# Performance work log

Hardware: AMD Instinct MI355X
Metric: run time of the kernel (lower is better)

The kernel has to match this reference:

```python
import jax, jax.numpy as jnp
import numpy as np

N, E, F_IN, H, C = 50000, 800000, 128, 64, 10

def setup_inputs() -> dict:
    key = jax.random.key(0)
    ks = jax.random.split(key, 8)
    x = jax.random.normal(ks[0], (N, F_IN), dtype=jnp.float32)
    edge_index = jax.random.randint(ks[1], (2, E), 0, N, dtype=jnp.int32)
    edge_weight = jax.random.uniform(ks[2], (E,), dtype=jnp.float32)
    W1 = jax.random.normal(ks[3], (H, F_IN), dtype=jnp.float32) * 0.05
    W2 = jax.random.normal(ks[4], (H, H), dtype=jnp.float32) * 0.05
    W3 = jax.random.normal(ks[5], (C, H), dtype=jnp.float32) * 0.05
    b1 = jnp.zeros((H,), jnp.float32)
    b2 = jnp.zeros((H,), jnp.float32)
    b3 = jnp.zeros((C,), jnp.float32)
    return {"x": x, "edge_index": edge_index, "edge_weight": edge_weight,
            "W1": W1, "b1": b1, "W2": W2, "b2": b2, "W3": W3, "b3": b3}

def reference(x, edge_index, edge_weight, W1, b1, W2, b2, W3, b3):
    n = x.shape[0]
    row, col = edge_index[0], edge_index[1]
    # GCN symmetric normalization (add_self_loops=False): deg from edge weights on col
    deg = jax.ops.segment_sum(edge_weight, col, num_segments=n)  # [N]
    dinv = jnp.where(deg > 0, jax.lax.rsqrt(deg), 0.0)
    norm = dinv[row] * edge_weight * dinv[col]  # [E]

    def gcn_layer(h, W, b):
        h = h @ W.T                               # linear transform [N, out]
        msg = h[row] * norm[:, None]              # gather + scale   [E, out]
        agg = jax.ops.segment_sum(msg, col, num_segments=n)  # scatter-add [N, out]
        return agg + b

    h = gcn_layer(x, W1, b1)
    h = gcn_layer(h, W2, b2)
    logits = gcn_layer(h, W3, b3)
    soft = jax.nn.softmax(logits, axis=1)
    return logits, soft
```

## Files before the change

kernel.cpp:

```cpp
#include <hip/hip_runtime.h>
#include <hip/hip_fp16.h>

#define N_NODES 50000
#define N_EDGES 800000
#define F_IN    128
#define H_DIM   64
#define C_DIM   10
#define CPAD    16
#define CAP     48
#define BLOCK   256
#define BIN_NODES 256
#define NBINS   196
#define QN      64
#define STRIDE  4480
#define E_BLK   2048
#define ABLOCKS ((N_EDGES + E_BLK - 1) / E_BLK)
#define DGB     (N_NODES / 16)
#define WB      ((N_NODES * 64) / 256)
#define POISON  ((int)0xAAAAAAAA)

__device__ __forceinline__ int unbase(int v) {
    return ((unsigned)v < 65536u) ? v : v - POISON;
}

__device__ __forceinline__ int   prow(unsigned v) { return (int)(v >> 16); }
__device__ __forceinline__ float pw(unsigned v)   {
    return __half2float(__ushort_as_half((unsigned short)(v & 0xFFFFu)));
}

__global__ __launch_bounds__(256) void k_binA(const int* __restrict__ rows,
                                              const int* __restrict__ cols,
                                              const float* __restrict__ ew,
                                              const float* __restrict__ W1,
                                              const float* __restrict__ b1,
                                              const float* __restrict__ W2,
                                              const float* __restrict__ b2,
                                              const float* __restrict__ W3,
                                              int* __restrict__ bucketCnt,
                                              unsigned* __restrict__ regionA,
                                              unsigned short* __restrict__ regionC,
                                              float* __restrict__ T2g,
                                              float* __restrict__ v1g,
                                              float* __restrict__ v2g) {
    const int tid = threadIdx.x;
    if (blockIdx.x < ABLOCKS) {
        __shared__ unsigned       sA[E_BLK];
        __shared__ unsigned short sC[E_BLK];
        __shared__ int hcnt[NBINS];
        __shared__ int lbase[NBINS];
        __shared__ int gb[NBINS];
        for (int i = tid; i < NBINS; i += BLOCK) hcnt[i] = 0;
        __syncthreads();

        const int e0 = blockIdx.x * E_BLK;
        unsigned rw[8];
        unsigned cl[8];
#pragma unroll
        for (int j = 0; j < 8; ++j) {
            int e = e0 + j * BLOCK + tid;
            if (e < N_EDGES) {
                int   c = cols[e];
                int   r = rows[e];
                float w = ew[e];
                rw[j] = ((unsigned)r << 16) | (unsigned)__half_as_ushort(__float2half(w));
                int lr = atomicAdd(&hcnt[c >> 8], 1);
                cl[j] = (unsigned)c | ((unsigned)lr << 16);
            } else {
                cl[j] = 0xFFFFFFFFu;
            }
        }
        __syncthreads();

        if (tid < 64) {
            int run = 0;
            for (int base = 0; base < NBINS; base += 64) {
                int i = base + tid;
                int v = (i < NBINS) ? hcnt[i] : 0;
                int s = v;
#pragma unroll
                for (int off = 1; off < 64; off <<= 1) {
                    int t = __shfl_up(s, off);
                    if (tid >= off) s += t;
                }
                if (i < NBINS) lbase[i] = run + s - v;
                run += __shfl(s, 63);
            }
        }
        __syncthreads();

#pragma unroll
        for (int j = 0; j < 8; ++j) {
            if (cl[j] != 0xFFFFFFFFu) {
                int c  = (int)(cl[j] & 0xFFFFu);
                int lr = (int)(cl[j] >> 16);
                int pos = lbase[c >> 8] + lr;
                sA[pos] = rw[j];
                sC[pos] = (unsigned short)c;
            }
        }
        if (tid < NBINS && hcnt[tid] > 0)
            gb[tid] = unbase(atomicAdd(&bucketCnt[tid], hcnt[tid]));
        __syncthreads();

        const int total = lbase[NBINS - 1] + hcnt[NBINS - 1];
        for (int i = tid; i < total; i += BLOCK) {
            int c = sC[i];
            int b = c >> 8;
            int gpos = gb[b] + (i - lbase[b]);
            if (gpos < STRIDE) {
                size_t p = (size_t)b * STRIDE + gpos;
                regionA[p] = sA[i];
                regionC[p] = (unsigned short)c;
            }
        }
        return;
    }

    __shared__ float u[C_DIM * H_DIM];
    for (int idx = tid; idx < C_DIM * H_DIM; idx += BLOCK) {
        int c = idx >> 6, j = idx & 63;
        float a = 0.f;
#pragma unroll
        for (int k = 0; k < H_DIM; ++k) a += W3[c * H_DIM + k] * W2[k * H_DIM + j];
        u[idx] = a;
    }
    __syncthreads();
    for (int idx = tid; idx < C_DIM * F_IN; idx += BLOCK) {
        int c = idx >> 7, f = idx & 127;
        float a = 0.f;
#pragma unroll
        for (int k = 0; k < H_DIM; ++k) a += u[c * H_DIM + k] * W1[k * F_IN + f];
        T2g[idx] = a;
    }
    if (tid < C_DIM) {
        float a = 0.f, b = 0.f;
#pragma unroll
        for (int k = 0; k < H_DIM; ++k) {
            a += u[tid * H_DIM + k] * b1[k];
            b += W3[tid * H_DIM + k] * b2[k];
        }
        v1g[tid] = a;
        v2g[tid] = b;
    }
}

__global__ __launch_bounds__(256) void k_binB(const int* __restrict__ bucketCnt,
                                              const unsigned* __restrict__ regionA,
                                              const unsigned short* __restrict__ regionC,
                                              float2* __restrict__ meta,
                                              unsigned* __restrict__ edata) {
    __shared__ unsigned sdata[QN * CAP];
    __shared__ int   lcnt[QN];
    __shared__ float wsum[QN];
    const int tid = threadIdx.x;
    const int b   = blockIdx.x >> 2;
    const int q   = blockIdx.x & 3;
    const int n0  = b * BIN_NODES + q * QN;
    if (n0 >= N_NODES) return;
    if (tid < QN) { lcnt[tid] = 0; wsum[tid] = 0.f; }
    __syncthreads();

    int tot = unbase(bucketCnt[b]);
    if (tot > STRIDE) tot = STRIDE;
    const size_t segBase = (size_t)b * STRIDE;
    const int lo = q * QN, hi = lo + QN;
    for (int i = tid; i < tot; i += BLOCK) {
        int cl = (int)regionC[segBase + i] - b * BIN_NODES;
        unsigned e = regionA[segBase + i];
        if (cl >= lo && cl < hi) {
            int nl = cl - lo;
            int r = atomicAdd(&lcnt[nl], 1);
            if (r < CAP) sdata[nl * CAP + r] = e;
            atomicAdd(&wsum[nl], pw(e));
        }
    }
    __syncthreads();

    const int nvalid = min(N_NODES - n0, QN);
    if (tid < nvalid) {
        int c0 = min(lcnt[tid], CAP);
        int cp = (c0 + 15) & ~15;
        if (cp > CAP) cp = CAP;
        for (int r = c0; r < cp; ++r) sdata[tid * CAP + r] = 0u;
        float d = wsum[tid];
        meta[n0 + tid] = make_float2(d > 0.f ? rsqrtf(d) : 0.f, (float)cp);
    }
    __syncthreads();

    int4* dst = reinterpret_cast<int4*>(edata + (size_t)n0 * CAP);
    const int4* src = reinterpret_cast<const int4*>(sdata);
    const int nvec = nvalid * (CAP / 4);
    for (int i = tid; i < nvec; i += BLOCK) dst[i] = src[i];
}

__global__ __launch_bounds__(256) void k_dg(const float* __restrict__ x,
                                            const float* __restrict__ T2g,
                                            const float2* __restrict__ meta,
                                            __half* __restrict__ bufA) {
    __shared__ float ts[16 * 132];
    __shared__ float xs[16][132];
    const int tid = threadIdx.x;
    const int n0 = blockIdx.x * 16;

    for (int i = tid; i < 16 * F_IN; i += BLOCK) {
        int c = i >> 7;
        ts[c * 132 + (i & 127)] = (c < C_DIM) ? T2g[i] : 0.f;
    }
    for (int i = tid; i < 16 * 32; i += BLOCK) {
        int ln = i >> 5, f4 = i & 31;
        float4 v = reinterpret_cast<const float4*>(x)[(n0 + ln) * 32 + f4];
        *reinterpret_cast<float4*>(&xs[ln][f4 * 4]) = v;
    }
    __syncthreads();

    const int g = tid >> 4;
    const int c = tid & 15;
    const int n = n0 + g;
    const float di = meta[n].x;

    const float4* tsv = reinterpret_cast<const float4*>(&ts[c * 132]);
    const float4* xv  = reinterpret_cast<const float4*>(&xs[g][0]);
    float a = 0.f;
#pragma unroll 8
    for (int f4 = 0; f4 < 32; ++f4) {
        float4 xx = xv[f4], tt = tsv[f4];
        a += xx.x * tt.x + xx.y * tt.y + xx.z * tt.z + xx.w * tt.w;
    }
    float outv = (c < C_DIM) ? a * di : (c == 10 ? di : 0.f);
    bufA[n * CPAD + c] = __float2half(outv);
}

__global__ __launch_bounds__(256) void k_gather(const float2* __restrict__ meta,
                                                const unsigned* __restrict__ edata,
                                                const __half* __restrict__ zin,
                                                __half* __restrict__ zout) {
    int n = (blockIdx.x * 256 + threadIdx.x) >> 6;
    if (n >= N_NODES) return;
    const int lane = threadIdx.x & 63;
    const int sub = lane >> 3;
    const int c2  = lane & 7;
    float2 m = meta[n];
    const float di = m.x;
    const int iters = ((int)m.y) >> 4;
    const uint2* bp = reinterpret_cast<const uint2*>(edata + n * CAP) + sub;
    float ax = 0.f, ay = 0.f;
#pragma unroll
    for (int i = 0; i < 3; ++i) {
        if (i < iters) {
            uint2 e = bp[i * 8];
            {
                float2 z = __half22float2(
                    reinterpret_cast<const __half2*>(zin + prow(e.x) * CPAD)[c2]);
                float w = pw(e.x);
                ax += w * z.x; ay += w * z.y;
            }
            {
                float2 z = __half22float2(
                    reinterpret_cast<const __half2*>(zin + prow(e.y) * CPAD)[c2]);
                float w = pw(e.y);
                ax += w * z.x; ay += w * z.y;
            }
        }
    }
    ax += __shfl_xor(ax, 8);  ay += __shfl_xor(ay, 8);
    ax += __shfl_xor(ax, 16); ay += __shfl_xor(ay, 16);
    ax += __shfl_xor(ax, 32); ay += __shfl_xor(ay, 32);
    if (lane < 8) {
        float s = di * di;
        reinterpret_cast<__half2*>(zout + n * CPAD)[lane] =
            __floats2half2_rn(ax * s, ay * s);
    }
}

__global__ __launch_bounds__(256) void k_final(const float2* __restrict__ meta,
                                               const unsigned* __restrict__ edata,
                                               const __half* __restrict__ zin,
                                               const __half* __restrict__ s1buf,
                                               const float* __restrict__ v1,
                                               const float* __restrict__ v2,
                                               const float* __restrict__ b3,
                                               float* __restrict__ logits,
                                               float* __restrict__ soft) {
    int n = (blockIdx.x * 256 + threadIdx.x) >> 6;
    if (n >= N_NODES) return;
    const int lane = threadIdx.x & 63;
    const int sub = lane >> 3;
    const int c2  = lane & 7;
    float2 m = meta[n];
    const float di = m.x;
    const int iters = ((int)m.y) >> 4;
    const uint2* bp = reinterpret_cast<const uint2*>(edata + n * CAP) + sub;
    float ax = 0.f, ay = 0.f;
#pragma unroll
    for (int i = 0; i < 3; ++i) {
        if (i < iters) {
            uint2 e = bp[i * 8];
            {
                float2 z = __half22float2(
                    reinterpret_cast<const __half2*>(zin + prow(e.x) * CPAD)[c2]);
                float w = pw(e.x);
                ax += w * z.x; ay += w * z.y;
            }
            {
                float2 z = __half22float2(
                    reinterpret_cast<const __half2*>(zin + prow(e.y) * CPAD)[c2]);
                float w = pw(e.y);
                ax += w * z.x; ay += w * z.y;
            }
        }
    }
    ax += __shfl_xor(ax, 8);  ay += __shfl_xor(ay, 8);
    ax += __shfl_xor(ax, 16); ay += __shfl_xor(ay, 16);
    ax += __shfl_xor(ax, 32); ay += __shfl_xor(ay, 32);

    const float r  = di > 0.f ? 1.0f / di : 0.f;
    const float a1 = __half2float(s1buf[n * CPAD + 10]) * r;
    const float a2 = __half2float(zin[n * CPAD + 10]) * r;
    float l0 = -1e30f, l1 = -1e30f;
    if (c2 < 5) {
        float2 w1 = reinterpret_cast<const float2*>(v1)[c2];
        float2 w2 = reinterpret_cast<const float2*>(v2)[c2];
        float2 bb = reinterpret_cast<const float2*>(b3)[c2];
        l0 = di * ax + a2 * w1.x + a1 * w2.x + bb.x;
        l1 = di * ay + a2 * w1.y + a1 * w2.y + bb.y;
    }
    float mx = fmaxf(l0, l1);
    mx = fmaxf(mx, __shfl_xor(mx, 1));
    mx = fmaxf(mx, __shfl_xor(mx, 2));
    mx = fmaxf(mx, __shfl_xor(mx, 4));
    float e0 = (c2 < 5) ? __expf(l0 - mx) : 0.f;
    float e1 = (c2 < 5) ? __expf(l1 - mx) : 0.f;
    float s = e0 + e1;
    s += __shfl_xor(s, 1);
    s += __shfl_xor(s, 2);
    s += __shfl_xor(s, 4);
    if (lane < 5) {
        float inv = 1.0f / s;
        reinterpret_cast<float2*>(logits + (size_t)n * C_DIM)[lane] = make_float2(l0, l1);
        reinterpret_cast<float2*>(soft   + (size_t)n * C_DIM)[lane] = make_float2(e0 * inv, e1 * inv);
    }
}

extern "C" void kernel_launch(void* const* d_in, const int* in_sizes, int n_in,
                              void* d_out, int out_size, void* d_ws, size_t ws_size,
                              hipStream_t stream) {
    const float* x  = (const float*)d_in[0];
    const int*   ei = (const int*)d_in[1];
    const float* ew = (const float*)d_in[2];
    const float* W1 = (const float*)d_in[3];
    const float* b1 = (const float*)d_in[4];
    const float* W2 = (const float*)d_in[5];
    const float* b2 = (const float*)d_in[6];
    const float* W3 = (const float*)d_in[7];
    const float* b3 = (const float*)d_in[8];
    const int* rows = ei;
    const int* cols = ei + N_EDGES;

    char* ws = (char*)d_ws;
    size_t off = 0;
    auto alloc = [&](size_t bytes) { void* q = ws + off; off += (bytes + 15) & ~size_t(15); return q; };

    float2*         meta      = (float2*)         alloc((size_t)N_NODES * 8);
    __half*         bufA      = (__half*)         alloc((size_t)N_NODES * CPAD * 2);
    __half*         bufB      = (__half*)         alloc((size_t)N_NODES * CPAD * 2);
    float*          T2g       = (float*)          alloc(C_DIM * F_IN * 4);
    float*          v1        = (float*)          alloc(64);
    float*          v2        = (float*)          alloc(64);
    int*            bucketCnt = (int*)            alloc(NBINS * 4);
    unsigned*       regionA   = (unsigned*)       alloc((size_t)NBINS * STRIDE * 4);
    unsigned short* regionC   = (unsigned short*) alloc((size_t)NBINS * STRIDE * 2);
    unsigned*       edata     = (unsigned*)       alloc((size_t)N_NODES * CAP * 4);

    float* logits = (float*)d_out;
    float* soft   = logits + N_NODES * C_DIM;

    k_binA<<<ABLOCKS + 1, BLOCK, 0, stream>>>(rows, cols, ew, W1, b1, W2, b2, W3,
                                              bucketCnt, regionA, regionC, T2g, v1, v2);
    k_binB<<<NBINS * 4, BLOCK, 0, stream>>>(bucketCnt, regionA, regionC, meta, edata);
    k_dg<<<DGB, BLOCK, 0, stream>>>(x, T2g, meta, bufA);
    k_gather<<<WB, BLOCK, 0, stream>>>(meta, edata, bufA, bufB);
    k_gather<<<WB, BLOCK, 0, stream>>>(meta, edata, bufB, bufA);
    k_final<<<WB, BLOCK, 0, stream>>>(meta, edata, bufA, bufB, v1, v2, b3,
                                      logits, soft);
}
```

Baseline: 167.9 us.

## Fuse feature projection into binning kernel and grid-stride gather kernels

Moves the x·T2 projection (former k_dg) into k_binB, so each bin block computes the projected features for its 64 nodes using the dinv it just computed in shared memory. This removes one kernel launch and the meta re-read. Separately, the gather and final kernels switch from one wave per node to a fixed 2048-block grid-stride loop, which cuts block scheduling overhead. The cost is extra shared memory and serial work per binB block, which may reduce occupancy in that kernel.

```diff
diff --git a/kernel.cpp b/kernel.cpp
--- a/kernel.cpp
+++ b/kernel.cpp
@@ -15,8 +15,8 @@
 #define STRIDE  4480
 #define E_BLK   2048
 #define ABLOCKS ((N_EDGES + E_BLK - 1) / E_BLK)
-#define DGB     (N_NODES / 16)
-#define WB      ((N_NODES * 64) / 256)
+#define GBLK    2048
+#define NWAVES  (GBLK * 4)
 #define POISON  ((int)0xAAAAAAAA)
 
 __device__ __forceinline__ int unbase(int v) {
@@ -147,17 +147,27 @@
 __global__ __launch_bounds__(256) void k_binB(const int* __restrict__ bucketCnt,
                                               const unsigned* __restrict__ regionA,
                                               const unsigned short* __restrict__ regionC,
+                                              const float* __restrict__ x,
+                                              const float* __restrict__ T2g,
                                               float2* __restrict__ meta,
-                                              unsigned* __restrict__ edata) {
+                                              unsigned* __restrict__ edata,
+                                              __half* __restrict__ bufA) {
     __shared__ unsigned sdata[QN * CAP];
     __shared__ int   lcnt[QN];
     __shared__ float wsum[QN];
+    __shared__ float dinvs[QN];
+    __shared__ float ts[16 * 132];
+    __shared__ float xs[16][132];
     const int tid = threadIdx.x;
     const int b   = blockIdx.x >> 2;
     const int q   = blockIdx.x & 3;
     const int n0  = b * BIN_NODES + q * QN;
     if (n0 >= N_NODES) return;
     if (tid < QN) { lcnt[tid] = 0; wsum[tid] = 0.f; }
+    for (int i = tid; i < 16 * F_IN; i += BLOCK) {
+        int c = i >> 7;
+        ts[c * 132 + (i & 127)] = (c < C_DIM) ? T2g[i] : 0.f;
+    }
     __syncthreads();
 
     int tot = unbase(bucketCnt[b]);
@@ -183,92 +193,88 @@
         if (cp > CAP) cp = CAP;
         for (int r = c0; r < cp; ++r) sdata[tid * CAP + r] = 0u;
         float d = wsum[tid];
-        meta[n0 + tid] = make_float2(d > 0.f ? rsqrtf(d) : 0.f, (float)cp);
+        float di = d > 0.f ? rsqrtf(d) : 0.f;
+        dinvs[tid] = di;
+        meta[n0 + tid] = make_float2(di, (float)cp);
     }
     __syncthreads();
 
-    int4* dst = reinterpret_cast<int4*>(edata + (size_t)n0 * CAP);
-    const int4* src = reinterpret_cast<const int4*>(sdata);
-    const int nvec = nvalid * (CAP / 4);
-    for (int i = tid; i < nvec; i += BLOCK) dst[i] = src[i];
-}
-
-__global__ __launch_bounds__(256) void k_dg(const float* __restrict__ x,
-                                            const float* __restrict__ T2g,
-                                            const float2* __restrict__ meta,
-                                            __half* __restrict__ bufA) {
-    __shared__ float ts[16 * 132];
-    __shared__ float xs[16][132];
-    const int tid = threadIdx.x;
-    const int n0 = blockIdx.x * 16;
-
-    for (int i = tid; i < 16 * F_IN; i += BLOCK) {
-        int c = i >> 7;
-        ts[c * 132 + (i & 127)] = (c < C_DIM) ? T2g[i] : 0.f;
-    }
-    for (int i = tid; i < 16 * 32; i += BLOCK) {
-        int ln = i >> 5, f4 = i & 31;
-        float4 v = reinterpret_cast<const float4*>(x)[(n0 + ln) * 32 + f4];
-        *reinterpret_cast<float4*>(&xs[ln][f4 * 4]) = v;
-    }
-    __syncthreads();
-
-    const int g = tid >> 4;
-    const int c = tid & 15;
-    const int n = n0 + g;
-    const float di = meta[n].x;
-
-    const float4* tsv = reinterpret_cast<const float4*>(&ts[c * 132]);
-    const float4* xv  = reinterpret_cast<const float4*>(&xs[g][0]);
-    float a = 0.f;
+    {
+        int4* dst = reinterpret_cast<int4*>(edata + (size_t)n0 * CAP);
+        const int4* src = reinterpret_cast<const int4*>(sdata);
+        const int nvec = nvalid * (CAP / 4);
+        for (int i = tid; i < nvec; i += BLOCK) dst[i] = src[i];
+    }
+
+    const int g = tid >> 4, c = tid & 15;
+    for (int t = 0; t < QN / 16; ++t) {
+        __syncthreads();
+        const int n0t = n0 + t * 16;
+        for (int i = tid; i < 16 * 32; i += BLOCK) {
+            int ln = i >> 5, f4 = i & 31;
+            if (n0t + ln < N_NODES) {
+                float4 v = reinterpret_cast<const float4*>(x)[(n0t + ln) * 32 + f4];
+                *reinterpret_cast<float4*>(&xs[ln][f4 * 4]) = v;
+            }
+        }
+        __syncthreads();
+        const int n = n0t + g;
+        if (n < N_NODES) {
+            const float di = dinvs[t * 16 + g];
+            const float4* tsv = reinterpret_cast<const float4*>(&ts[c * 132]);
+            const float4* xv  = reinterpret_cast<const float4*>(&xs[g][0]);
+            float a = 0.f;
 #pragma unroll 8
-    for (int f4 = 0; f4 < 32; ++f4) {
-        float4 xx = xv[f4], tt = tsv[f4];
-        a += xx.x * tt.x + xx.y * tt.y + xx.z * tt.z + xx.w * tt.w;
-    }
-    float outv = (c < C_DIM) ? a * di : (c == 10 ? di : 0.f);
-    bufA[n * CPAD + c] = __float2half(outv);
+            for (int f4 = 0; f4 < 32; ++f4) {
+                float4 xx = xv[f4], tt = tsv[f4];
+                a += xx.x * tt.x + xx.y * tt.y + xx.z * tt.z + xx.w * tt.w;
+            }
+            float outv = (c < C_DIM) ? a * di : (c == 10 ? di : 0.f);
+            bufA[n * CPAD + c] = __float2half(outv);
+        }
+    }
 }
 
 __global__ __launch_bounds__(256) void k_gather(const float2* __restrict__ meta,
                                                 const unsigned* __restrict__ edata,
                                                 const __half* __restrict__ zin,
                                                 __half* __restrict__ zout) {
-    int n = (blockIdx.x * 256 + threadIdx.x) >> 6;
-    if (n >= N_NODES) return;
     const int lane = threadIdx.x & 63;
     const int sub = lane >> 3;
     const int c2  = lane & 7;
-    float2 m = meta[n];
-    const float di = m.x;
-    const int iters = ((int)m.y) >> 4;
-    const uint2* bp = reinterpret_cast<const uint2*>(edata + n * CAP) + sub;
-    float ax = 0.f, ay = 0.f;
-#pragma unroll
-    for (int i = 0; i < 3; ++i) {
-        if (i < iters) {
-            uint2 e = bp[i * 8];
-            {
-                float2 z = __half22float2(
-                    reinterpret_cast<const __half2*>(zin + prow(e.x) * CPAD)[c2]);
-                float w = pw(e.x);
-                ax += w * z.x; ay += w * z.y;
-            }
-            {
-                float2 z = __half22float2(
-                    reinterpret_cast<const __half2*>(zin + prow(e.y) * CPAD)[c2]);
-                float w = pw(e.y);
-                ax += w * z.x; ay += w * z.y;
-            }
-        }
-    }
-    ax += __shfl_xor(ax, 8);  ay += __shfl_xor(ay, 8);
-    ax += __shfl_xor(ax, 16); ay += __shfl_xor(ay, 16);
-    ax += __shfl_xor(ax, 32); ay += __shfl_xor(ay, 32);
-    if (lane < 8) {
-        float s = di * di;
-        reinterpret_cast<__half2*>(zout + n * CPAD)[lane] =
-            __floats2half2_rn(ax * s, ay * s);
+    const int w0 = (blockIdx.x * 256 + threadIdx.x) >> 6;
+    for (int n = w0; n < N_NODES; n += NWAVES) {
+        float2 m = meta[n];
+        const float di = m.x;
+        const int iters = ((int)m.y) >> 4;
+        const uint2* bp = reinterpret_cast<const uint2*>(edata + n * CAP) + sub;
+        float ax = 0.f, ay = 0.f;
+#pragma unroll
+        for (int i = 0; i < 3; ++i) {
+            if (i < iters) {
+                uint2 e = bp[i * 8];
+                {
+                    float2 z = __half22float2(
+                        reinterpret_cast<const __half2*>(zin + prow(e.x) * CPAD)[c2]);
+                    float w = pw(e.x);
+                    ax += w * z.x; ay += w * z.y;
+                }
+                {
+                    float2 z = __half22float2(
+                        reinterpret_cast<const __half2*>(zin + prow(e.y) * CPAD)[c2]);
+                    float w = pw(e.y);
+                    ax += w * z.x; ay += w * z.y;
+                }
+            }
+        }
+        ax += __shfl_xor(ax, 8);  ay += __shfl_xor(ay, 8);
+        ax += __shfl_xor(ax, 16); ay += __shfl_xor(ay, 16);
+        ax += __shfl_xor(ax, 32); ay += __shfl_xor(ay, 32);
+        if (lane < 8) {
+            float s = di * di;
+            reinterpret_cast<__half2*>(zout + n * CPAD)[lane] =
+                __floats2half2_rn(ax * s, ay * s);
+        }
     }
 }
 
@@ -281,63 +287,64 @@
                                                const float* __restrict__ b3,
                                                float* __restrict__ logits,
                                                float* __restrict__ soft) {
-    int n = (blockIdx.x * 256 + threadIdx.x) >> 6;
-    if (n >= N_NODES) return;
     const int lane = threadIdx.x & 63;
     const int sub = lane >> 3;
     const int c2  = lane & 7;
-    float2 m = meta[n];
-    const float di = m.x;
-    const int iters = ((int)m.y) >> 4;
-    const uint2* bp = reinterpret_cast<const uint2*>(edata + n * CAP) + sub;
-    float ax = 0.f, ay = 0.f;
-#pragma unroll
-    for (int i = 0; i < 3; ++i) {
-        if (i < iters) {
-            uint2 e = bp[i * 8];
-            {
-                float2 z = __half22float2(
-                    reinterpret_cast<const __half2*>(zin + prow(e.x) * CPAD)[c2]);
-                float w = pw(e.x);
-                ax += w * z.x; ay += w * z.y;
-            }
-            {
-                float2 z = __half22float2(
-                    reinterpret_cast<const __half2*>(zin + prow(e.y) * CPAD)[c2]);
-                float w = pw(e.y);
-                ax += w * z.x; ay += w * z.y;
-            }
-        }
-    }
-    ax += __shfl_xor(ax, 8);  ay += __shfl_xor(ay, 8);
-    ax += __shfl_xor(ax, 16); ay += __shfl_xor(ay, 16);
-    ax += __shfl_xor(ax, 32); ay += __shfl_xor(ay, 32);
-
-    const float r  = di > 0.f ? 1.0f / di : 0.f;
-    const float a1 = __half2float(s1buf[n * CPAD + 10]) * r;
-    const float a2 = __half2float(zin[n * CPAD + 10]) * r;
-    float l0 = -1e30f, l1 = -1e30f;
-    if (c2 < 5) {
-        float2 w1 = reinterpret_cast<const float2*>(v1)[c2];
-        float2 w2 = reinterpret_cast<const float2*>(v2)[c2];
-        float2 bb = reinterpret_cast<const float2*>(b3)[c2];
-        l0 = di * ax + a2 * w1.x + a1 * w2.x + bb.x;
-        l1 = di * ay + a2 * w1.y + a1 * w2.y + bb.y;
-    }
-    float mx = fmaxf(l0, l1);
-    mx = fmaxf(mx, __shfl_xor(mx, 1));
-    mx = fmaxf(mx, __shfl_xor(mx, 2));
-    mx = fmaxf(mx, __shfl_xor(mx, 4));
-    float e0 = (c2 < 5) ? __expf(l0 - mx) : 0.f;
-    float e1 = (c2 < 5) ? __expf(l1 - mx) : 0.f;
-    float s = e0 + e1;
-    s += __shfl_xor(s, 1);
-    s += __shfl_xor(s, 2);
-    s += __shfl_xor(s, 4);
-    if (lane < 5) {
-        float inv = 1.0f / s;
-        reinterpret_cast<float2*>(logits + (size_t)n * C_DIM)[lane] = make_float2(l0, l1);
-        reinterpret_cast<float2*>(soft   + (size_t)n * C_DIM)[lane] = make_float2(e0 * inv, e1 * inv);
+    const int w0 = (blockIdx.x * 256 + threadIdx.x) >> 6;
+    for (int n = w0; n < N_NODES; n += NWAVES) {
+        float2 m = meta[n];
+        const float di = m.x;
+        const int iters = ((int)m.y) >> 4;
+        const uint2* bp = reinterpret_cast<const uint2*>(edata + n * CAP) + sub;
+        float ax = 0.f, ay = 0.f;
+#pragma unroll
+        for (int i = 0; i < 3; ++i) {
+            if (i < iters) {
+                uint2 e = bp[i * 8];
+                {
+                    float2 z = __half22float2(
+                        reinterpret_cast<const __half2*>(zin + prow(e.x) * CPAD)[c2]);
+                    float w = pw(e.x);
+                    ax += w * z.x; ay += w * z.y;
+                }
+                {
+                    float2 z = __half22float2(
+                        reinterpret_cast<const __half2*>(zin + prow(e.y) * CPAD)[c2]);
+                    float w = pw(e.y);
+                    ax += w * z.x; ay += w * z.y;
+                }
+            }
+        }
+        ax += __shfl_xor(ax, 8);  ay += __shfl_xor(ay, 8);
+        ax += __shfl_xor(ax, 16); ay += __shfl_xor(ay, 16);
+        ax += __shfl_xor(ax, 32); ay += __shfl_xor(ay, 32);
+
+        const float r  = di > 0.f ? 1.0f / di : 0.f;
+        const float a1 = __half2float(s1buf[n * CPAD + 10]) * r;
+        const float a2 = __half2float(zin[n * CPAD + 10]) * r;
+        float l0 = -1e30f, l1 = -1e30f;
+        if (c2 < 5) {
+            float2 w1 = reinterpret_cast<const float2*>(v1)[c2];
+            float2 w2 = reinterpret_cast<const float2*>(v2)[c2];
+            float2 bb = reinterpret_cast<const float2*>(b3)[c2];
+            l0 = di * ax + a2 * w1.x + a1 * w2.x + bb.x;
+            l1 = di * ay + a2 * w1.y + a1 * w2.y + bb.y;
+        }
+        float mx = fmaxf(l0, l1);
+        mx = fmaxf(mx, __shfl_xor(mx, 1));
+        mx = fmaxf(mx, __shfl_xor(mx, 2));
+        mx = fmaxf(mx, __shfl_xor(mx, 4));
+        float e0 = (c2 < 5) ? __expf(l0 - mx) : 0.f;
+        float e1 = (c2 < 5) ? __expf(l1 - mx) : 0.f;
+        float s = e0 + e1;
+        s += __shfl_xor(s, 1);
+        s += __shfl_xor(s, 2);
+        s += __shfl_xor(s, 4);
+        if (lane < 5) {
+            float inv = 1.0f / s;
+            reinterpret_cast<float2*>(logits + (size_t)n * C_DIM)[lane] = make_float2(l0, l1);
+            reinterpret_cast<float2*>(soft   + (size_t)n * C_DIM)[lane] = make_float2(e0 * inv, e1 * inv);
+        }
     }
 }
 
@@ -376,10 +383,10 @@
 
     k_binA<<<ABLOCKS + 1, BLOCK, 0, stream>>>(rows, cols, ew, W1, b1, W2, b2, W3,
                                               bucketCnt, regionA, regionC, T2g, v1, v2);
-    k_binB<<<NBINS * 4, BLOCK, 0, stream>>>(bucketCnt, regionA, regionC, meta, edata);
-    k_dg<<<DGB, BLOCK, 0, stream>>>(x, T2g, meta, bufA);
-    k_gather<<<WB, BLOCK, 0, stream>>>(meta, edata, bufA, bufB);
-    k_gather<<<WB, BLOCK, 0, stream>>>(meta, edata, bufB, bufA);
-    k_final<<<WB, BLOCK, 0, stream>>>(meta, edata, bufA, bufB, v1, v2, b3,
-                                      logits, soft);
-}
+    k_binB<<<NBINS * 4, BLOCK, 0, stream>>>(bucketCnt, regionA, regionC, x, T2g,
+                                            meta, edata, bufA);
+    k_gather<<<GBLK, BLOCK, 0, stream>>>(meta, edata, bufA, bufB);
+    k_gather<<<GBLK, BLOCK, 0, stream>>>(meta, edata, bufB, bufA);
+    k_final<<<GBLK, BLOCK, 0, stream>>>(meta, edata, bufA, bufB, v1, v2, b3,
+                                        logits, soft);
+}
```

After: 163.0 us. -2.9%, faster.
